# Optimization experiments

Measured on AMD Instinct MI355X. Metric: run time of the kernel, lower is better.

## Reference

```python
import jax, jax.numpy as jnp
import numpy as np

CLAMP_MIN = 1e-6
CLAMP_MAX = 1e6


def setup_inputs() -> dict:
    key = jax.random.key(0)
    k1, k2, k3, k4, k5 = jax.random.split(key, 5)
    R, F, K = 4096, 256, 8
    return {
        "x1": jax.random.normal(k1, (R, F), dtype=jnp.float32),
        "x2": jax.random.normal(k2, (R, F), dtype=jnp.float32),
        "sigmas": jax.random.normal(k3, (K,), dtype=jnp.float32) * 100.0,
        "means": jax.random.normal(k4, (K,), dtype=jnp.float32),
        "sigma_parameters": jax.random.normal(k5, (K,), dtype=jnp.float32),
    }


def reference(x1, x2, sigmas, means, sigma_parameters):
    # dist_k[i,j] = sum_f (x1[i,f] - x2[j,f] - mean_k)^2
    #            = ||x1_i - x2_j||^2 - 2*mean_k*sum_f(x1_i - x2_j) + F*mean_k^2
    # Expansion avoids materializing the R x R x F broadcast tensor.
    R, F = x1.shape
    base = (
        jnp.sum(x1 * x1, axis=1)[:, None]
        + jnp.sum(x2 * x2, axis=1)[None, :]
        - 2.0 * (x1 @ x2.T)
    )  # [R, R]
    s = jnp.sum(x1, axis=1)[:, None] - jnp.sum(x2, axis=1)[None, :]  # [R, R]

    mean = means[:, None, None]  # [K,1,1]
    dist = base[None] - 2.0 * mean * s[None] + jnp.float32(F) * mean * mean  # [K,R,R]
    dist = jnp.clip(dist, CLAMP_MIN, CLAMP_MAX)

    kernel_value = jnp.exp(-dist / (2.0 * sigmas[:, None, None] ** 2))  # [K,R,R]
    softmaxed = jax.nn.softmax(kernel_value, axis=2)  # torch softmax(dim=1) per [R,R]

    weights = 1.0 / (sigma_parameters ** 2)
    normalized_weights = jax.nn.softmax(weights)  # softmax over K
    return jnp.sum(softmaxed * normalized_weights[:, None, None], axis=0)  # [R, R]
```

## Files before the change

kernel.cpp:

```cpp
#include <hip/hip_runtime.h>
#include <cmath>

#define R 4096
#define F 256
#define NK 8

typedef _Float16 half8 __attribute__((ext_vector_type(8)));
typedef _Float16 half4v __attribute__((ext_vector_type(4)));
typedef float f32x4 __attribute__((ext_vector_type(4)));

#define LOG2E 1.4426950408889634f


__global__ __launch_bounds__(256) void prep_kernel(
    const float* __restrict__ x1, const float* __restrict__ x2,
    const float* __restrict__ sigmas, const float* __restrict__ means,
    const float* __restrict__ sigp,
    _Float16* __restrict__ x1h, _Float16* __restrict__ x2h,
    float* __restrict__ r1, float* __restrict__ sq1,
    float* __restrict__ r2, float* __restrict__ sq2,
    float* __restrict__ S, float* __restrict__ prm)
{
    const int tid  = threadIdx.x;
    const int wid  = tid >> 6;
    const int lane = tid & 63;
    const int row  = blockIdx.x * 4 + wid;

    const float* src; _Float16* dsth; float* rs; float* rq; int r;
    if (row < R) { src = x1; dsth = x1h; rs = r1; rq = sq1; r = row; }
    else         { src = x2; dsth = x2h; rs = r2; rq = sq2; r = row - R; }

    float4 v = ((const float4*)(src + (size_t)r * F))[lane];
    half4v h = { (_Float16)v.x, (_Float16)v.y, (_Float16)v.z, (_Float16)v.w };
    *(half4v*)(dsth + (size_t)r * F + lane * 4) = h;

    float s = v.x + v.y + v.z + v.w;
    float q = v.x * v.x + v.y * v.y + v.z * v.z + v.w * v.w;
    for (int m = 1; m < 64; m <<= 1) {
        s += __shfl_xor(s, m);
        q += __shfl_xor(q, m);
    }
    if (lane == 0) { rs[r] = s; rq[r] = q; }

    int g = blockIdx.x * 256 + tid;
    if (g < NK * R) S[g] = 0.f;

    if (blockIdx.x == 0 && tid == 0) {
        float w[NK], mx = -1e30f;
        for (int k = 0; k < NK; ++k) { float sp = sigp[k]; w[k] = 1.f / (sp * sp); mx = fmaxf(mx, w[k]); }
        float sum = 0.f;
        for (int k = 0; k < NK; ++k) { w[k] = expf(w[k] - mx); sum += w[k]; }
        for (int k = 0; k < NK; ++k) prm[k] = w[k] / sum;
        for (int k = 0; k < NK; ++k) { float sg = sigmas[k]; prm[8 + k] = 1.f / (2.f * sg * sg); }
        for (int k = 0; k < NK; ++k) { float m = means[k]; prm[16 + k] = 2.f * m; prm[24 + k] = (float)F * m * m; }
    }
}

__global__ __launch_bounds__(256) void finalize_kernel(
    float* __restrict__ S, const float* __restrict__ prm)
{
    int g = blockIdx.x * 256 + threadIdx.x;
    int k = g >> 12;
    S[g] = prm[k] / S[g];
}

template <int PHASE>
__global__ __launch_bounds__(256, 2) void gemm_kernel(
    const _Float16* __restrict__ Ah, const _Float16* __restrict__ Bh,
    const float* __restrict__ r1, const float* __restrict__ sq1,
    const float* __restrict__ r2, const float* __restrict__ sq2,
    const float* __restrict__ prm, float* __restrict__ S, float* __restrict__ out)
{
    constexpr int SK = 72;
    __shared__ _Float16 As[128 * SK];
    __shared__ _Float16 Bs[128 * SK];

    const int tid  = threadIdx.x;
    const int lane = tid & 63;
    const int wid  = tid >> 6;
    const int wm   = wid >> 1, wn = wid & 1;
    const int q    = lane >> 4, m16 = lane & 15;
    const int tm   = blockIdx.y, tn = blockIdx.x;

    f32x4 acc[4][4];
#pragma unroll
    for (int a = 0; a < 4; ++a)
#pragma unroll
        for (int b = 0; b < 4; ++b)
            acc[a][b] = (f32x4){0.f, 0.f, 0.f, 0.f};

    for (int k0 = 0; k0 < F; k0 += 64) {
#pragma unroll
        for (int c = 0; c < 4; ++c) {
            int idx = c * 256 + tid;
            int row = idx >> 3, c8 = (idx & 7) * 8;
            *(uint4*)&As[row * SK + c8] =
                *(const uint4*)&Ah[(size_t)(tm * 128 + row) * F + k0 + c8];
            *(uint4*)&Bs[row * SK + c8] =
                *(const uint4*)&Bh[(size_t)(tn * 128 + row) * F + k0 + c8];
        }
        __syncthreads();
#pragma unroll
        for (int s = 0; s < 2; ++s) {
            half8 a[4], b[4];
#pragma unroll
            for (int mt = 0; mt < 4; ++mt)
                a[mt] = *(const half8*)&As[(wm * 64 + mt * 16 + m16) * SK + s * 32 + q * 8];
#pragma unroll
            for (int nt = 0; nt < 4; ++nt)
                b[nt] = *(const half8*)&Bs[(wn * 64 + nt * 16 + m16) * SK + s * 32 + q * 8];
#pragma unroll
            for (int mt = 0; mt < 4; ++mt)
#pragma unroll
                for (int nt = 0; nt < 4; ++nt)
                    acc[mt][nt] = __builtin_amdgcn_mfma_f32_16x16x32_f16(
                        a[mt], b[nt], acc[mt][nt], 0, 0, 0);
        }
        __syncthreads();
    }

    int colg[4]; float c2[4], cr[4];
#pragma unroll
    for (int nt = 0; nt < 4; ++nt) {
        colg[nt] = tn * 128 + wn * 64 + nt * 16 + m16;
        c2[nt] = sq2[colg[nt]];
        cr[nt] = r2[colg[nt]];
    }
    float colk[8][4];
#pragma unroll
    for (int k = 0; k < 8; ++k) {
        float twoM = prm[16 + k];
#pragma unroll
        for (int nt = 0; nt < 4; ++nt) colk[k][nt] = c2[nt] + twoM * cr[nt];
    }

    if (PHASE == 0) {
#pragma unroll
        for (int mt = 0; mt < 4; ++mt) {
#pragma unroll
            for (int r = 0; r < 4; ++r) {
                int rowg = tm * 128 + wm * 64 + mt * 16 + q * 4 + r;
                float rq2 = sq1[rowg], rr = r1[rowg];
#pragma unroll
                for (int k = 0; k < 8; ++k) {
                    float is2  = prm[8 + k];
                    float twoM = prm[16 + k];
                    float m2F  = prm[24 + k];
                    float nis2 = -is2;
                    float rowa = rq2 - twoM * rr + m2F;
                    float t = 0.f;
#pragma unroll
                    for (int nt = 0; nt < 4; ++nt) {
                        float dist = rowa + colk[k][nt] - 2.f * acc[mt][nt][r];
                        dist = fminf(fmaxf(dist, 1e-6f), 1e6f);
                        t += __expf(__expf(dist * nis2));
                    }
                    t += __shfl_xor(t, 1); t += __shfl_xor(t, 2);
                    t += __shfl_xor(t, 4); t += __shfl_xor(t, 8);
                    if (m16 == 0) atomicAdd(&S[k * R + rowg], t);
                }
            }
        }
    } else {
#pragma unroll
        for (int mt = 0; mt < 4; ++mt) {
#pragma unroll
            for (int r = 0; r < 4; ++r) {
                int rowg = tm * 128 + wm * 64 + mt * 16 + q * 4 + r;
                float rq2 = sq1[rowg], rr = r1[rowg];
                float rowa[8], sv[8];
#pragma unroll
                for (int k = 0; k < 8; ++k) {
                    rowa[k] = rq2 - prm[16 + k] * rr + prm[24 + k];
                    sv[k]   = S[k * R + rowg];
                }
#pragma unroll
                for (int nt = 0; nt < 4; ++nt) {
                    float d2 = 2.f * acc[mt][nt][r];
                    float o = 0.f;
#pragma unroll
                    for (int k = 0; k < 8; ++k) {
                        float dist = rowa[k] + colk[k][nt] - d2;
                        dist = fminf(fmaxf(dist, 1e-6f), 1e6f);
                        o += sv[k] * __expf(__expf(dist * -prm[8 + k]));
                    }
                    __builtin_nontemporal_store(o, &out[(size_t)rowg * R + colg[nt]]);
                }
            }
        }
    }
}

extern "C" void kernel_launch(void* const* d_in, const int* in_sizes, int n_in,
                              void* d_out, int out_size, void* d_ws, size_t ws_size,
                              hipStream_t stream) {
    (void)in_sizes; (void)n_in; (void)out_size; (void)ws_size;
    const float* x1     = (const float*)d_in[0];
    const float* x2     = (const float*)d_in[1];
    const float* sigmas = (const float*)d_in[2];
    const float* means  = (const float*)d_in[3];
    const float* sigp   = (const float*)d_in[4];
    float* out = (float*)d_out;

    char* ws = (char*)d_ws;
    _Float16* x1h = (_Float16*)ws;
    _Float16* x2h = (_Float16*)(ws + 2097152);
    float* r1  = (float*)(ws + 4194304);
    float* sq1 = (float*)(ws + 4194304 + 16384);
    float* r2  = (float*)(ws + 4194304 + 32768);
    float* sq2 = (float*)(ws + 4194304 + 49152);
    float* S   = (float*)(ws + 4194304 + 65536);
    float* prm = (float*)(ws + 4194304 + 65536 + 131072);

    prep_kernel<<<2048, 256, 0, stream>>>(x1, x2, sigmas, means, sigp,
                                          x1h, x2h, r1, sq1, r2, sq2, S, prm);
    gemm_kernel<0><<<dim3(32, 32), 256, 0, stream>>>(x1h, x2h, r1, sq1, r2, sq2, prm, S, out);
    finalize_kernel<<<128, 256, 0, stream>>>(S, prm);
    gemm_kernel<1><<<dim3(32, 32), 256, 0, stream>>>(x1h, x2h, r1, sq1, r2, sq2, prm, S, out);
}
```

Before: 199.8 us.

## Fold per-row/column distance terms into exp2 arguments and shrink GEMM tile rows

```diff
diff --git a/kernel.cpp b/kernel.cpp
--- a/kernel.cpp
+++ b/kernel.cpp
@@ -9,13 +9,13 @@
 typedef _Float16 half4v __attribute__((ext_vector_type(4)));
 typedef float f32x4 __attribute__((ext_vector_type(4)));
 
-#define LOG2E 1.4426950408889634f
+#define LOG2E      1.4426950408889634f
+#define LOG2LOG2E  0.5287663729448977f
 
 
 __global__ __launch_bounds__(256) void prep_kernel(
     const float* __restrict__ x1, const float* __restrict__ x2,
-    const float* __restrict__ sigmas, const float* __restrict__ means,
-    const float* __restrict__ sigp,
+    const float* __restrict__ sigmas, const float* __restrict__ sigp,
     _Float16* __restrict__ x1h, _Float16* __restrict__ x2h,
     float* __restrict__ r1, float* __restrict__ sq1,
     float* __restrict__ r2, float* __restrict__ sq2,
@@ -51,9 +51,30 @@
         float sum = 0.f;
         for (int k = 0; k < NK; ++k) { w[k] = expf(w[k] - mx); sum += w[k]; }
         for (int k = 0; k < NK; ++k) prm[k] = w[k] / sum;
-        for (int k = 0; k < NK; ++k) { float sg = sigmas[k]; prm[8 + k] = 1.f / (2.f * sg * sg); }
-        for (int k = 0; k < NK; ++k) { float m = means[k]; prm[16 + k] = 2.f * m; prm[24 + k] = (float)F * m * m; }
-    }
+        for (int k = 0; k < NK; ++k) {
+            float sg = sigmas[k];
+            float is2 = 1.f / (2.f * sg * sg);
+            prm[8 + k] = 2.f * is2 * LOG2E;
+        }
+    }
+}
+
+__global__ __launch_bounds__(256) void prep2_kernel(
+    const float* __restrict__ sigmas, const float* __restrict__ means,
+    const float* __restrict__ r1, const float* __restrict__ sq1,
+    const float* __restrict__ r2, const float* __restrict__ sq2,
+    float* __restrict__ rA, float* __restrict__ cB)
+{
+    int idx  = blockIdx.x * 256 + threadIdx.x;
+    int half = idx >> 15;
+    int k    = (idx >> 12) & 7;
+    int i    = idx & 4095;
+    float sg = sigmas[k], m = means[k];
+    float c  = -LOG2E / (2.f * sg * sg);
+    if (half == 0)
+        rA[k * R + i] = c * (sq1[i] - 2.f * m * r1[i] + (float)F * m * m) + LOG2LOG2E;
+    else
+        cB[k * R + i] = c * (sq2[i] + 2.f * m * r2[i]);
 }
 
 __global__ __launch_bounds__(256) void finalize_kernel(
@@ -65,15 +86,16 @@
 }
 
 template <int PHASE>
-__global__ __launch_bounds__(256, 2) void gemm_kernel(
+__global__ __launch_bounds__(256, 4) void gemm_kernel(
     const _Float16* __restrict__ Ah, const _Float16* __restrict__ Bh,
-    const float* __restrict__ r1, const float* __restrict__ sq1,
-    const float* __restrict__ r2, const float* __restrict__ sq2,
+    const float* __restrict__ rA, const float* __restrict__ cB,
     const float* __restrict__ prm, float* __restrict__ S, float* __restrict__ out)
 {
     constexpr int SK = 72;
-    __shared__ _Float16 As[128 * SK];
+    __shared__ _Float16 As[64 * SK];
     __shared__ _Float16 Bs[128 * SK];
+    float* rowSt = (float*)As;
+    float* colSt = (float*)Bs;
 
     const int tid  = threadIdx.x;
     const int lane = tid & 63;
@@ -82,35 +104,43 @@
     const int q    = lane >> 4, m16 = lane & 15;
     const int tm   = blockIdx.y, tn = blockIdx.x;
 
-    f32x4 acc[4][4];
-#pragma unroll
-    for (int a = 0; a < 4; ++a)
+    f32x4 acc[2][4];
+#pragma unroll
+    for (int a = 0; a < 2; ++a)
 #pragma unroll
         for (int b = 0; b < 4; ++b)
             acc[a][b] = (f32x4){0.f, 0.f, 0.f, 0.f};
 
+    const size_t abase = (size_t)(tm * 64) * F;
+    const size_t bbase = (size_t)(tn * 128) * F;
+
     for (int k0 = 0; k0 < F; k0 += 64) {
+#pragma unroll
+        for (int c = 0; c < 2; ++c) {
+            int idx = c * 256 + tid;
+            int row = idx >> 3, c8 = (idx & 7) * 8;
+            *(uint4*)&As[row * SK + c8] =
+                *(const uint4*)&Ah[abase + (size_t)row * F + k0 + c8];
+        }
 #pragma unroll
         for (int c = 0; c < 4; ++c) {
             int idx = c * 256 + tid;
             int row = idx >> 3, c8 = (idx & 7) * 8;
-            *(uint4*)&As[row * SK + c8] =
-                *(const uint4*)&Ah[(size_t)(tm * 128 + row) * F + k0 + c8];
             *(uint4*)&Bs[row * SK + c8] =
-                *(const uint4*)&Bh[(size_t)(tn * 128 + row) * F + k0 + c8];
+                *(const uint4*)&Bh[bbase + (size_t)row * F + k0 + c8];
         }
         __syncthreads();
 #pragma unroll
         for (int s = 0; s < 2; ++s) {
-            half8 a[4], b[4];
-#pragma unroll
-            for (int mt = 0; mt < 4; ++mt)
-                a[mt] = *(const half8*)&As[(wm * 64 + mt * 16 + m16) * SK + s * 32 + q * 8];
+            half8 a[2], b[4];
+#pragma unroll
+            for (int mt = 0; mt < 2; ++mt)
+                a[mt] = *(const half8*)&As[(wm * 32 + mt * 16 + m16) * SK + s * 32 + q * 8];
 #pragma unroll
             for (int nt = 0; nt < 4; ++nt)
                 b[nt] = *(const half8*)&Bs[(wn * 64 + nt * 16 + m16) * SK + s * 32 + q * 8];
 #pragma unroll
-            for (int mt = 0; mt < 4; ++mt)
+            for (int mt = 0; mt < 2; ++mt)
 #pragma unroll
                 for (int nt = 0; nt < 4; ++nt)
                     acc[mt][nt] = __builtin_amdgcn_mfma_f32_16x16x32_f16(
@@ -119,72 +149,80 @@
         __syncthreads();
     }
 
-    int colg[4]; float c2[4], cr[4];
+#pragma unroll
+    for (int c = 0; c < 4; ++c) {
+        int id2 = c * 256 + tid;
+        int row = id2 >> 4, slot = id2 & 15;
+        float v;
+        if (slot < 8) v = rA[slot * R + tm * 64 + row];
+        else          v = (PHASE == 1) ? S[(slot - 8) * R + tm * 64 + row] : 0.f;
+        rowSt[row * 17 + slot] = v;
+    }
+#pragma unroll
+    for (int c = 0; c < 4; ++c) {
+        int id2 = c * 256 + tid;
+        int col = id2 >> 3, k = id2 & 7;
+        colSt[col * 9 + k] = cB[k * R + tn * 128 + col];
+    }
+    __syncthreads();
+
+    float g[8];
+#pragma unroll
+    for (int k = 0; k < 8; ++k) g[k] = prm[8 + k];
+
+    float colQ[4][8];
 #pragma unroll
     for (int nt = 0; nt < 4; ++nt) {
-        colg[nt] = tn * 128 + wn * 64 + nt * 16 + m16;
-        c2[nt] = sq2[colg[nt]];
-        cr[nt] = r2[colg[nt]];
-    }
-    float colk[8][4];
-#pragma unroll
-    for (int k = 0; k < 8; ++k) {
-        float twoM = prm[16 + k];
-#pragma unroll
-        for (int nt = 0; nt < 4; ++nt) colk[k][nt] = c2[nt] + twoM * cr[nt];
-    }
-
-    if (PHASE == 0) {
-#pragma unroll
-        for (int mt = 0; mt < 4; ++mt) {
-#pragma unroll
-            for (int r = 0; r < 4; ++r) {
-                int rowg = tm * 128 + wm * 64 + mt * 16 + q * 4 + r;
-                float rq2 = sq1[rowg], rr = r1[rowg];
+        int col = wn * 64 + nt * 16 + m16;
+#pragma unroll
+        for (int k = 0; k < 8; ++k) colQ[nt][k] = colSt[col * 9 + k];
+    }
+
+#pragma unroll
+    for (int mt = 0; mt < 2; ++mt) {
+#pragma unroll
+        for (int r = 0; r < 4; ++r) {
+            int rowl = wm * 32 + mt * 16 + q * 4 + r;
+            float rAv[8];
+#pragma unroll
+            for (int k = 0; k < 8; ++k) rAv[k] = rowSt[rowl * 17 + k];
+
+            if (PHASE == 0) {
+                float tk[8];
+#pragma unroll
+                for (int k = 0; k < 8; ++k) tk[k] = 0.f;
+#pragma unroll
+                for (int nt = 0; nt < 4; ++nt) {
+                    float d = acc[mt][nt][r];
+#pragma unroll
+                    for (int k = 0; k < 8; ++k) {
+                        float t = fmaf(g[k], d, rAv[k] + colQ[nt][k]);
+                        tk[k] += __builtin_amdgcn_exp2f(__builtin_amdgcn_exp2f(t));
+                    }
+                }
 #pragma unroll
                 for (int k = 0; k < 8; ++k) {
-                    float is2  = prm[8 + k];
-                    float twoM = prm[16 + k];
-                    float m2F  = prm[24 + k];
-                    float nis2 = -is2;
-                    float rowa = rq2 - twoM * rr + m2F;
-                    float t = 0.f;
-#pragma unroll
-                    for (int nt = 0; nt < 4; ++nt) {
-                        float dist = rowa + colk[k][nt] - 2.f * acc[mt][nt][r];
-                        dist = fminf(fmaxf(dist, 1e-6f), 1e6f);
-                        t += __expf(__expf(dist * nis2));
-                    }
+                    float t = tk[k];
                     t += __shfl_xor(t, 1); t += __shfl_xor(t, 2);
                     t += __shfl_xor(t, 4); t += __shfl_xor(t, 8);
-                    if (m16 == 0) atomicAdd(&S[k * R + rowg], t);
+                    if (m16 == 0) atomicAdd(&S[k * R + tm * 64 + rowl], t);
                 }
-            }
-        }
-    } else {
-#pragma unroll
-        for (int mt = 0; mt < 4; ++mt) {
-#pragma unroll
-            for (int r = 0; r < 4; ++r) {
-                int rowg = tm * 128 + wm * 64 + mt * 16 + q * 4 + r;
-                float rq2 = sq1[rowg], rr = r1[rowg];
-                float rowa[8], sv[8];
-#pragma unroll
-                for (int k = 0; k < 8; ++k) {
-                    rowa[k] = rq2 - prm[16 + k] * rr + prm[24 + k];
-                    sv[k]   = S[k * R + rowg];
-                }
+            } else {
+                float sv[8];
+#pragma unroll
+                for (int k = 0; k < 8; ++k) sv[k] = rowSt[rowl * 17 + 8 + k];
+                int rowg = tm * 64 + rowl;
 #pragma unroll
                 for (int nt = 0; nt < 4; ++nt) {
-                    float d2 = 2.f * acc[mt][nt][r];
+                    float d = acc[mt][nt][r];
                     float o = 0.f;
 #pragma unroll
                     for (int k = 0; k < 8; ++k) {
-                        float dist = rowa[k] + colk[k][nt] - d2;
-                        dist = fminf(fmaxf(dist, 1e-6f), 1e6f);
-                        o += sv[k] * __expf(__expf(dist * -prm[8 + k]));
+                        float t = fmaf(g[k], d, rAv[k] + colQ[nt][k]);
+                        o = fmaf(sv[k], __builtin_amdgcn_exp2f(__builtin_amdgcn_exp2f(t)), o);
                     }
-                    __builtin_nontemporal_store(o, &out[(size_t)rowg * R + colg[nt]]);
+                    int colg = tn * 128 + wn * 64 + nt * 16 + m16;
+                    __builtin_nontemporal_store(o, &out[(size_t)rowg * R + colg]);
                 }
             }
         }
@@ -210,11 +248,14 @@
     float* r2  = (float*)(ws + 4194304 + 32768);
     float* sq2 = (float*)(ws + 4194304 + 49152);
     float* S   = (float*)(ws + 4194304 + 65536);
-    float* prm = (float*)(ws + 4194304 + 65536 + 131072);
-
-    prep_kernel<<<2048, 256, 0, stream>>>(x1, x2, sigmas, means, sigp,
+    float* rA  = (float*)(ws + 4194304 + 196608);
+    float* cB  = (float*)(ws + 4194304 + 327680);
+    float* prm = (float*)(ws + 4194304 + 458752);
+
+    prep_kernel<<<2048, 256, 0, stream>>>(x1, x2, sigmas, sigp,
                                           x1h, x2h, r1, sq1, r2, sq2, S, prm);
-    gemm_kernel<0><<<dim3(32, 32), 256, 0, stream>>>(x1h, x2h, r1, sq1, r2, sq2, prm, S, out);
+    prep2_kernel<<<256, 256, 0, stream>>>(sigmas, means, r1, sq1, r2, sq2, rA, cB);
+    gemm_kernel<0><<<dim3(32, 64), 256, 0, stream>>>(x1h, x2h, rA, cB, prm, S, out);
     finalize_kernel<<<128, 256, 0, stream>>>(S, prm);
-    gemm_kernel<1><<<dim3(32, 32), 256, 0, stream>>>(x1h, x2h, r1, sq1, r2, sq2, prm, S, out);
-}
+    gemm_kernel<1><<<dim3(32, 64), 256, 0, stream>>>(x1h, x2h, rA, cB, prm, S, out);
+}
```

After: 207.4 us. 1.04x slower.
